# Kernel tuning notes

Hardware: AMD Instinct MI355X
Metric: run time of the kernel (lower is better)

The kernel has to match this reference:

```python
import jax, jax.numpy as jnp
import numpy as np

ALPHA = 0.2          # LeakyReLU negative slope
WIN = 100            # window_size
D_EMBED = 2 * WIN    # default d_embed doubled in __init__


def setup_inputs() -> dict:
    key = jax.random.key(0)
    k1, k2, k3, k4 = jax.random.split(key, 4)
    B, W, F = 16, WIN, 128
    inp = jax.random.normal(k1, (B, W, F), dtype=jnp.float32)
    # linear: in=2*window_size, out=d_embed (stored as [in, out] for x @ W)
    lim = np.sqrt(1.0 / (2 * WIN))
    lin_w = jax.random.uniform(k2, (2 * WIN, D_EMBED), jnp.float32, -lim, lim)
    lin_b = jax.random.uniform(k3, (D_EMBED,), jnp.float32, -lim, lim)
    # attention vector w: [d_embed] (xavier on [d_embed,1])
    glim = np.sqrt(6.0 / (D_EMBED + 1))
    attn_w = jax.random.uniform(k4, (D_EMBED,), jnp.float32, -glim, glim)
    return {"input": inp, "lin_w": lin_w, "lin_b": lin_b, "attn_w": attn_w}


def reference(input, lin_w, lin_b, attn_w):
    # input: [B, window, features] -> x: [B, K, window] (K = features = nodes)
    x = jnp.transpose(input, (0, 2, 1))
    # Split the linear over the concat: linear(cat(xi, xj)) = xi@W1 + xj@W2 + b
    W1, W2 = lin_w[:WIN], lin_w[WIN:]          # each [window, d_embed]
    left = jnp.einsum("bkw,wd->bkd", x, W1)    # [B, K, d]
    right = jnp.einsum("bkw,wd->bkd", x, W2)   # [B, K, d]
    pre = left[:, :, None, :] + right[:, None, :, :] + lin_b  # [B, K, K, d]
    act = jnp.where(pre >= 0, pre, ALPHA * pre)                # LeakyReLU
    e = jnp.einsum("bijd,d->bij", act, attn_w)                 # [B, K, K]
    attention = jax.nn.softmax(e, axis=2)
    # dropout p=0.0 (eval/identity)
    h = jax.nn.sigmoid(jnp.einsum("bij,bjw->biw", attention, x))  # [B, K, window]
    return jnp.transpose(h, (0, 2, 1))  # [B, window, K]
```

## Files before the change

### kernel.cpp

```cpp
#include <hip/hip_runtime.h>

#define ALPHA 0.2f
#define BATCH 16
#define WIN 100
#define KN 128
#define DE 200
#define IT 8

typedef float v2f __attribute__((ext_vector_type(2)));

__global__ __launch_bounds__(256) void k_lin(
    const float* __restrict__ in, const float* __restrict__ lw,
    const float* __restrict__ lb, float* __restrict__ Rt, float* __restrict__ Lt) {
  int blk = blockIdx.x;
  int b = blk / 25, dt = blk % 25;
  int t = threadIdx.x;
  int j = t & (KN - 1);
  int dbase = __builtin_amdgcn_readfirstlane(dt * 8 + (t >> 7) * 4);
  const float* inb = in + (size_t)b * WIN * KN + j;
  const float* lwl = lw + dbase;
  const float* lwr = lw + WIN * DE + dbase;
  float la0 = 0, la1 = 0, la2 = 0, la3 = 0;
  float ra0 = 0, ra1 = 0, ra2 = 0, ra3 = 0;
#pragma unroll 10
  for (int w = 0; w < WIN; ++w) {
    float x = inb[w * KN];
    float4 wl = *reinterpret_cast<const float4*>(lwl + w * DE);
    float4 wr = *reinterpret_cast<const float4*>(lwr + w * DE);
    la0 = fmaf(x, wl.x, la0); la1 = fmaf(x, wl.y, la1);
    la2 = fmaf(x, wl.z, la2); la3 = fmaf(x, wl.w, la3);
    ra0 = fmaf(x, wr.x, ra0); ra1 = fmaf(x, wr.y, ra1);
    ra2 = fmaf(x, wr.z, ra2); ra3 = fmaf(x, wr.w, ra3);
  }
  float4 bb = *reinterpret_cast<const float4*>(lb + dbase);
  float* rp = Rt + ((size_t)b * DE + dbase) * KN + j;
  float* lp = Lt + ((size_t)b * DE + dbase) * KN + j;
  rp[0 * KN] = ra0 + bb.x; rp[1 * KN] = ra1 + bb.y;
  rp[2 * KN] = ra2 + bb.z; rp[3 * KN] = ra3 + bb.w;
  lp[0 * KN] = la0; lp[1 * KN] = la1; lp[2 * KN] = la2; lp[3 * KN] = la3;
}

__global__ __launch_bounds__(1024) void k_attn_out(
    const float* __restrict__ in, const float* __restrict__ aw,
    const float* __restrict__ Rt, const float* __restrict__ Lt,
    float* __restrict__ out) {
  int blk = blockIdx.x;
  int b = blk >> 4, it = blk & 15;
  int i0 = it * IT;
  int t = threadIdx.x;
  __shared__ float Lis[DE][IT];
  __shared__ float aws[DE];
  __shared__ float part[8][IT][KN];
  __shared__ float part_r[8][KN];
  __shared__ float ats[IT][132];

  {
    const float* ltb = Lt + (size_t)b * DE * KN + i0;
    if (t < 2 * DE) {
      int d = t >> 1, h = (t & 1) << 2;
      *reinterpret_cast<float4*>(&Lis[d][h]) =
          *reinterpret_cast<const float4*>(ltb + (size_t)d * KN + h);
    }
    if (t >= 512 && t < 512 + DE) aws[t - 512] = aw[t - 512];
  }
  __syncthreads();

  {
    int j = t & (KN - 1);
    int dh = t >> 7;
    int db = __builtin_amdgcn_readfirstlane(dh * 25);
    const float* rtb = Rt + (size_t)b * DE * KN + j;
    v2f acc0 = 0.f, acc1 = 0.f, acc2 = 0.f, acc3 = 0.f;
    float racc = 0.f;
#pragma unroll 5
    for (int dd = 0; dd < 25; ++dd) {
      int d = db + dd;
      float r = rtb[(size_t)d * KN];
      float a = aws[d];
      float4 L0 = *reinterpret_cast<const float4*>(&Lis[d][0]);
      float4 L1 = *reinterpret_cast<const float4*>(&Lis[d][4]);
      racc = fmaf(r, a, racc);
      v2f rv = {r, r}, av = {a, a}, z = 0.f;
      v2f p0 = (v2f){L0.x, L0.y} + rv;
      v2f p1 = (v2f){L0.z, L0.w} + rv;
      v2f p2 = (v2f){L1.x, L1.y} + rv;
      v2f p3 = (v2f){L1.z, L1.w} + rv;
      p0 = __builtin_elementwise_min(p0, z);
      p1 = __builtin_elementwise_min(p1, z);
      p2 = __builtin_elementwise_min(p2, z);
      p3 = __builtin_elementwise_min(p3, z);
      acc0 += p0 * av; acc1 += p1 * av; acc2 += p2 * av; acc3 += p3 * av;
    }
    part[dh][0][j] = acc0.x; part[dh][1][j] = acc0.y;
    part[dh][2][j] = acc1.x; part[dh][3][j] = acc1.y;
    part[dh][4][j] = acc2.x; part[dh][5][j] = acc2.y;
    part[dh][6][j] = acc3.x; part[dh][7][j] = acc3.y;
    part_r[dh][j] = racc;
  }
  __syncthreads();

  {
    int wid = t >> 6;
    if (wid < IT) {
      int r = wid, l = t & 63;
      float ra0 = 0.f, ra1 = 0.f, m0 = 0.f, m1 = 0.f;
#pragma unroll
      for (int s = 0; s < 8; ++s) {
        ra0 += part_r[s][l];     ra1 += part_r[s][l + 64];
        m0  += part[s][r][l];    m1  += part[s][r][l + 64];
      }
      float e0 = fmaf(m0, -(1.f - ALPHA), ra0);
      float e1 = fmaf(m1, -(1.f - ALPHA), ra1);
      float m = fmaxf(e0, e1);
      for (int off = 32; off; off >>= 1) m = fmaxf(m, __shfl_xor(m, off));
      float p0 = __expf(e0 - m), p1 = __expf(e1 - m);
      float s2 = p0 + p1;
      for (int off = 32; off; off >>= 1) s2 += __shfl_xor(s2, off);
      float inv = 1.f / s2;
      ats[r][l] = p0 * inv;
      ats[r][l + 64] = p1 * inv;
    }
  }
  __syncthreads();

  if (t < 8 * WIN) {
    int w = t >> 3, q = t & 7;
    const float* xw = in + ((size_t)b * WIN + w) * KN;
    const float* ap = &ats[q][0];
    float s = 0.f;
#pragma unroll 8
    for (int jj = 0; jj < KN; jj += 4) {
      float4 x4 = *reinterpret_cast<const float4*>(xw + jj);
      float4 aa = *reinterpret_cast<const float4*>(ap + jj);
      s = fmaf(aa.x, x4.x, s); s = fmaf(aa.y, x4.y, s);
      s = fmaf(aa.z, x4.z, s); s = fmaf(aa.w, x4.w, s);
    }
    out[((size_t)b * WIN + w) * KN + i0 + q] = 1.f / (1.f + __expf(-s));
  }
}

extern "C" void kernel_launch(void* const* d_in, const int* in_sizes, int n_in,
                              void* d_out, int out_size, void* d_ws, size_t ws_size,
                              hipStream_t stream) {
  const float* in = (const float*)d_in[0];
  const float* lw = (const float*)d_in[1];
  const float* lb = (const float*)d_in[2];
  const float* aw = (const float*)d_in[3];
  float* out = (float*)d_out;

  float* Rt = (float*)d_ws;
  float* Lt = Rt + (size_t)BATCH * DE * KN;

  k_lin     <<<BATCH * 25, 256, 0, stream>>>(in, lw, lb, Rt, Lt);
  k_attn_out<<<BATCH * 16, 1024, 0, stream>>>(in, aw, Rt, Lt, out);
}
```

Measured before the change: 23.98 us.

## Compute left projection inside attention kernel instead of via workspace

The left half of the linear projection (x@W1) is no longer computed by the first kernel and written to a global workspace. Each attention block now computes the 8 rows it needs directly from the input and weights before the main loop. This removes half the first kernel's work and the Lt global write/read round trip. In exchange, each attention block runs a 100-long serial dot product for 1600 outputs with strided, poorly coalesced global loads, which lengthens its prologue.

New measurement: 30.58 us. 27.5% more time.

```diff
diff --git a/kernel.cpp b/kernel.cpp
--- a/kernel.cpp
+++ b/kernel.cpp
@@ -11,38 +11,31 @@
 
 __global__ __launch_bounds__(256) void k_lin(
     const float* __restrict__ in, const float* __restrict__ lw,
-    const float* __restrict__ lb, float* __restrict__ Rt, float* __restrict__ Lt) {
+    const float* __restrict__ lb, float* __restrict__ Rt) {
   int blk = blockIdx.x;
   int b = blk / 25, dt = blk % 25;
   int t = threadIdx.x;
   int j = t & (KN - 1);
   int dbase = __builtin_amdgcn_readfirstlane(dt * 8 + (t >> 7) * 4);
   const float* inb = in + (size_t)b * WIN * KN + j;
-  const float* lwl = lw + dbase;
   const float* lwr = lw + WIN * DE + dbase;
-  float la0 = 0, la1 = 0, la2 = 0, la3 = 0;
   float ra0 = 0, ra1 = 0, ra2 = 0, ra3 = 0;
 #pragma unroll 10
   for (int w = 0; w < WIN; ++w) {
     float x = inb[w * KN];
-    float4 wl = *reinterpret_cast<const float4*>(lwl + w * DE);
     float4 wr = *reinterpret_cast<const float4*>(lwr + w * DE);
-    la0 = fmaf(x, wl.x, la0); la1 = fmaf(x, wl.y, la1);
-    la2 = fmaf(x, wl.z, la2); la3 = fmaf(x, wl.w, la3);
     ra0 = fmaf(x, wr.x, ra0); ra1 = fmaf(x, wr.y, ra1);
     ra2 = fmaf(x, wr.z, ra2); ra3 = fmaf(x, wr.w, ra3);
   }
   float4 bb = *reinterpret_cast<const float4*>(lb + dbase);
   float* rp = Rt + ((size_t)b * DE + dbase) * KN + j;
-  float* lp = Lt + ((size_t)b * DE + dbase) * KN + j;
   rp[0 * KN] = ra0 + bb.x; rp[1 * KN] = ra1 + bb.y;
   rp[2 * KN] = ra2 + bb.z; rp[3 * KN] = ra3 + bb.w;
-  lp[0 * KN] = la0; lp[1 * KN] = la1; lp[2 * KN] = la2; lp[3 * KN] = la3;
 }
 
 __global__ __launch_bounds__(1024) void k_attn_out(
-    const float* __restrict__ in, const float* __restrict__ aw,
-    const float* __restrict__ Rt, const float* __restrict__ Lt,
+    const float* __restrict__ in, const float* __restrict__ lw,
+    const float* __restrict__ aw, const float* __restrict__ Rt,
     float* __restrict__ out) {
   int blk = blockIdx.x;
   int b = blk >> 4, it = blk & 15;
@@ -54,15 +47,18 @@
   __shared__ float part_r[8][KN];
   __shared__ float ats[IT][132];
 
-  {
-    const float* ltb = Lt + (size_t)b * DE * KN + i0;
-    if (t < 2 * DE) {
-      int d = t >> 1, h = (t & 1) << 2;
-      *reinterpret_cast<float4*>(&Lis[d][h]) =
-          *reinterpret_cast<const float4*>(ltb + (size_t)d * KN + h);
-    }
-    if (t >= 512 && t < 512 + DE) aws[t - 512] = aw[t - 512];
+  for (int idx = t; idx < IT * DE; idx += 1024) {
+    int ii = idx / DE;
+    int d = idx - ii * DE;
+    const float* xc = in + (size_t)b * WIN * KN + i0 + ii;
+    const float* lc = lw + d;
+    float a = 0.f;
+#pragma unroll 4
+    for (int w = 0; w < WIN; ++w)
+      a = fmaf(xc[w * KN], lc[w * DE], a);
+    Lis[d][ii] = a;
   }
+  if (t >= 1024 - DE) aws[t - (1024 - DE)] = aw[t - (1024 - DE)];
   __syncthreads();
 
   {
@@ -149,8 +145,7 @@
   float* out = (float*)d_out;
 
   float* Rt = (float*)d_ws;
-  float* Lt = Rt + (size_t)BATCH * DE * KN;
 
-  k_lin     <<<BATCH * 25, 256, 0, stream>>>(in, lw, lb, Rt, Lt);
-  k_attn_out<<<BATCH * 16, 1024, 0, stream>>>(in, aw, Rt, Lt, out);
+  k_lin     <<<BATCH * 25, 256, 0, stream>>>(in, lw, lb, Rt);
+  k_attn_out<<<BATCH * 16, 1024, 0, stream>>>(in, lw, aw, Rt, out);
 }
```

## Store R as float4-interleaved and read L and attention weights directly from global

Applied to the files above, without the earlier changes.

The R projection is now stored in an interleaved layout of four d values per float4 per node, so each thread does one vector store and one vector load per four d values instead of four scalar accesses. The attention kernel drops its shared-memory staging of L and the attention vector, plus the barrier that followed it, and reads them straight from global memory. These are wave-uniform broadcast loads that should hit in cache. The d loop is split strided across the eight thread groups, which now handle 50/8 quads each, so the groups get uneven amounts of work. The gain is an earlier start and fewer scalar memory operations, at the cost of more global and cache traffic for the L values.

After: 27.44 us. 14.4% more time.

```diff
diff --git a/kernel.cpp b/kernel.cpp
--- a/kernel.cpp
+++ b/kernel.cpp
@@ -6,6 +6,7 @@
 #define KN 128
 #define DE 200
 #define IT 8
+#define NQ 50
 
 typedef float v2f __attribute__((ext_vector_type(2)));
 
@@ -33,10 +34,10 @@
     ra2 = fmaf(x, wr.z, ra2); ra3 = fmaf(x, wr.w, ra3);
   }
   float4 bb = *reinterpret_cast<const float4*>(lb + dbase);
-  float* rp = Rt + ((size_t)b * DE + dbase) * KN + j;
+  float4* rq = reinterpret_cast<float4*>(Rt) +
+               ((size_t)b * NQ + (dbase >> 2)) * KN + j;
+  *rq = make_float4(ra0 + bb.x, ra1 + bb.y, ra2 + bb.z, ra3 + bb.w);
   float* lp = Lt + ((size_t)b * DE + dbase) * KN + j;
-  rp[0 * KN] = ra0 + bb.x; rp[1 * KN] = ra1 + bb.y;
-  rp[2 * KN] = ra2 + bb.z; rp[3 * KN] = ra3 + bb.w;
   lp[0 * KN] = la0; lp[1 * KN] = la1; lp[2 * KN] = la2; lp[3 * KN] = la3;
 }
 
@@ -48,49 +49,48 @@
   int b = blk >> 4, it = blk & 15;
   int i0 = it * IT;
   int t = threadIdx.x;
-  __shared__ float Lis[DE][IT];
-  __shared__ float aws[DE];
   __shared__ float part[8][IT][KN];
   __shared__ float part_r[8][KN];
   __shared__ float ats[IT][132];
 
   {
-    const float* ltb = Lt + (size_t)b * DE * KN + i0;
-    if (t < 2 * DE) {
-      int d = t >> 1, h = (t & 1) << 2;
-      *reinterpret_cast<float4*>(&Lis[d][h]) =
-          *reinterpret_cast<const float4*>(ltb + (size_t)d * KN + h);
-    }
-    if (t >= 512 && t < 512 + DE) aws[t - 512] = aw[t - 512];
-  }
-  __syncthreads();
-
-  {
     int j = t & (KN - 1);
     int dh = t >> 7;
-    int db = __builtin_amdgcn_readfirstlane(dh * 25);
-    const float* rtb = Rt + (size_t)b * DE * KN + j;
+    const float4* rtq = reinterpret_cast<const float4*>(Rt) +
+                        (size_t)b * NQ * KN + j;
+    const float* ltb = Lt + (size_t)b * DE * KN + i0;
     v2f acc0 = 0.f, acc1 = 0.f, acc2 = 0.f, acc3 = 0.f;
     float racc = 0.f;
-#pragma unroll 5
-    for (int dd = 0; dd < 25; ++dd) {
-      int d = db + dd;
-      float r = rtb[(size_t)d * KN];
-      float a = aws[d];
-      float4 L0 = *reinterpret_cast<const float4*>(&Lis[d][0]);
-      float4 L1 = *reinterpret_cast<const float4*>(&Lis[d][4]);
-      racc = fmaf(r, a, racc);
-      v2f rv = {r, r}, av = {a, a}, z = 0.f;
-      v2f p0 = (v2f){L0.x, L0.y} + rv;
-      v2f p1 = (v2f){L0.z, L0.w} + rv;
-      v2f p2 = (v2f){L1.x, L1.y} + rv;
-      v2f p3 = (v2f){L1.z, L1.w} + rv;
-      p0 = __builtin_elementwise_min(p0, z);
-      p1 = __builtin_elementwise_min(p1, z);
-      p2 = __builtin_elementwise_min(p2, z);
-      p3 = __builtin_elementwise_min(p3, z);
-      acc0 += p0 * av; acc1 += p1 * av; acc2 += p2 * av; acc3 += p3 * av;
+
+#define EDOT(rr, aa, dd)                                                     \
+    {                                                                        \
+      float4 L0 = *reinterpret_cast<const float4*>(ltb + (size_t)(dd) * KN); \
+      float4 L1 = *reinterpret_cast<const float4*>(ltb + (size_t)(dd) * KN + 4); \
+      racc = fmaf((rr), (aa), racc);                                         \
+      v2f rv = {(rr), (rr)}, av = {(aa), (aa)}, z = 0.f;                     \
+      v2f p0 = (v2f){L0.x, L0.y} + rv;                                       \
+      v2f p1 = (v2f){L0.z, L0.w} + rv;                                       \
+      v2f p2 = (v2f){L1.x, L1.y} + rv;                                       \
+      v2f p3 = (v2f){L1.z, L1.w} + rv;                                       \
+      p0 = __builtin_elementwise_min(p0, z);                                 \
+      p1 = __builtin_elementwise_min(p1, z);                                 \
+      p2 = __builtin_elementwise_min(p2, z);                                 \
+      p3 = __builtin_elementwise_min(p3, z);                                 \
+      acc0 += p0 * av; acc1 += p1 * av; acc2 += p2 * av; acc3 += p3 * av;    \
     }
+
+#pragma unroll 2
+    for (int q = dh; q < NQ; q += 8) {
+      float4 r4 = rtq[(size_t)q * KN];
+      float4 a4 = *reinterpret_cast<const float4*>(aw + q * 4);
+      int d0 = q * 4;
+      EDOT(r4.x, a4.x, d0 + 0)
+      EDOT(r4.y, a4.y, d0 + 1)
+      EDOT(r4.z, a4.z, d0 + 2)
+      EDOT(r4.w, a4.w, d0 + 3)
+    }
+#undef EDOT
+
     part[dh][0][j] = acc0.x; part[dh][1][j] = acc0.y;
     part[dh][2][j] = acc1.x; part[dh][3][j] = acc1.y;
     part[dh][4][j] = acc2.x; part[dh][5][j] = acc2.y;
```
